# Performance work log

Measured on AMD Instinct MI355X. Metric: run time of the kernel, lower is better.

## Reference

```python
import jax, jax.numpy as jnp
import numpy as np
import math

B, T, IN_DIM = 2, 2048, 512
D, NH, MULT, N_LAYER = 512, 8, 4, 3
N = D * MULT // NH  # per-head latent dim = 256
OUT_DIM = 512
THETA = 2 ** 16


def get_freqs(n):
    t = jnp.arange(n, dtype=jnp.float32)
    q = jnp.floor(t / 2.0) * 2.0  # quantize(q=2)
    return 1.0 / (THETA ** (q / n)) / (2.0 * math.pi)


def ln(x, eps=1e-5):
    mu = jnp.mean(x, axis=-1, keepdims=True)
    var = jnp.var(x, axis=-1, keepdims=True)
    return (x - mu) * jax.lax.rsqrt(var + eps)


def rope(phases, v):
    # phases: [T, N] broadcastable to v [B, nh, T, N]
    p = (phases % 1.0) * (2.0 * math.pi)
    pc, ps = jnp.cos(p), jnp.sin(p)
    # interleave rotate: out[..., 2i] = -v[..., 2i+1], out[..., 2i+1] = v[..., 2i]
    v_rot = jnp.stack((-v[..., 1::2], v[..., ::2]), axis=-1).reshape(v.shape)
    return v * pc + v_rot * ps


def setup_inputs() -> dict:
    key = jax.random.key(0)
    ks = jax.random.split(key, 8)
    std = 0.02
    return {
        "x": jax.random.normal(ks[0], (B, T, IN_DIM), dtype=jnp.float32),
        "w_in": jax.random.normal(ks[1], (IN_DIM, D), dtype=jnp.float32) * std,
        "b_in": jnp.zeros((D,), dtype=jnp.float32),
        "encoder": jax.random.normal(ks[2], (NH, D, N), dtype=jnp.float32) * std,
        "encoder_v": jax.random.normal(ks[3], (NH, D, N), dtype=jnp.float32) * std,
        "decoder": jax.random.normal(ks[4], (NH * N, D), dtype=jnp.float32) * std,
        "head_w": jax.random.normal(ks[5], (D, OUT_DIM), dtype=jnp.float32) * std,
        "head_b": jnp.zeros((OUT_DIM,), dtype=jnp.float32),
    }


def reference(x, w_in, b_in, encoder, encoder_v, decoder, head_w, head_b):
    freqs = get_freqs(N)  # [N]
    t_idx = jnp.arange(T, dtype=jnp.float32)
    phases = t_idx[:, None] * freqs[None, :]  # [T, N]
    # strict lower-triangular causal mask (tril diagonal=-1)
    mask = (jnp.arange(T)[:, None] > jnp.arange(T)[None, :])  # [T, T]
    dec = decoder.reshape(NH, N, D)

    xs = ln(x @ w_in + b_in)  # [B, T, D]
    for _ in range(N_LAYER):
        x_res = xs
        x_sparse = jax.nn.relu(jnp.einsum('btd,hdn->bhtn', xs, encoder))  # [B,nh,T,N]
        QR = rope(phases, x_sparse)
        scores = jnp.einsum('bhtn,bhsn->bhts', QR, QR)
        scores = jnp.where(mask, scores, 0.0)
        yKV = jnp.einsum('bhts,bsd->bhtd', scores, xs)  # V = x (head-broadcast)
        yKV = ln(yKV)
        y_sparse = jax.nn.relu(jnp.einsum('bhtd,hdn->bhtn', yKV, encoder_v))
        xy_sparse = x_sparse * y_sparse  # dropout p=0 -> identity
        yMLP = jnp.einsum('bhtn,hnd->btd', xy_sparse, dec)
        xs = ln(x_res + ln(yMLP))
    logits = xs @ head_w + head_b
    return logits
```

## Files before the change

kernel.cpp:

```cpp
#include <hip/hip_runtime.h>
#include <math.h>

constexpr int B_  = 2;
constexpr int T_  = 2048;
constexpr int D_  = 512;
constexpr int NH_ = 8;
constexpr int NL_ = 256;
constexpr int HN_ = NH_ * NL_;
constexpr int BT_ = B_ * T_;

typedef __bf16 v8bf __attribute__((ext_vector_type(8)));
typedef float  v4f  __attribute__((ext_vector_type(4)));
typedef unsigned short us8 __attribute__((ext_vector_type(8)));
typedef unsigned short us4 __attribute__((ext_vector_type(4)));

__device__ inline unsigned short f2b(float f) {
    union { float f; unsigned u; } v{f};
    unsigned r = v.u + 0x7FFF + ((v.u >> 16) & 1);
    return (unsigned short)(r >> 16);
}
__device__ inline float b2f(unsigned short u) {
    union { unsigned u; float f; } v{(unsigned)u << 16};
    return v.f;
}

__device__ __forceinline__ void g2l16(const void* g, void* l) {
    __builtin_amdgcn_global_load_lds(
        (const __attribute__((address_space(1))) void*)g,
        (__attribute__((address_space(3))) void*)l, 16, 0, 0);
}

#define TILE_IDS                                              \
    int tid = threadIdx.x;                                    \
    int lane = tid & 63, wid = tid >> 6;                      \
    int wm = (wid & 1) * 64, wn = (wid >> 1) * 64;            \
    int ln16 = lane & 15, q = lane >> 4;                      \
    int srl = lane >> 2, scl = (lane & 3) * 8;                \
    (void)wm; (void)wn;

#define T128_STAGE(Ab, lda, Bb, ldb, k0, buf)                 \
    _Pragma("unroll")                                         \
    for (int ci = 0; ci < 4; ++ci) {                          \
        int c = wid * 4 + ci;                                 \
        if (c < 8) {                                          \
            int r = c * 16 + srl;                             \
            g2l16(Ab + (long)r * lda + (k0) + scl,            \
                  (char*)As[buf] + c * 1024);                 \
        } else {                                              \
            int r = (c - 8) * 16 + srl;                       \
            g2l16(Bb + (long)r * ldb + (k0) + scl,            \
                  (char*)Bs[buf] + (c - 8) * 1024);           \
        }                                                     \
    }

#define TILE_MFMA(Asx, Bsx)                                   \
    {                                                         \
        v8bf af[4], bfr[4];                                   \
        _Pragma("unroll")                                     \
        for (int r = 0; r < 4; ++r)                           \
            af[r] = *(const v8bf*)&Asx[wm + r * 16 + ln16][q * 8]; \
        _Pragma("unroll")                                     \
        for (int c = 0; c < 4; ++c)                           \
            bfr[c] = *(const v8bf*)&Bsx[wn + c * 16 + ln16][q * 8]; \
        _Pragma("unroll")                                     \
        for (int r = 0; r < 4; ++r)                           \
            _Pragma("unroll")                                 \
            for (int c = 0; c < 4; ++c)                       \
                acc[r][c] = __builtin_amdgcn_mfma_f32_16x16x32_bf16( \
                    af[r], bfr[c], acc[r][c], 0, 0, 0);       \
    }

template <int KS, bool RELU, bool MUL, bool BF16OUT, bool LNA>
__global__ __launch_bounds__(256) void gemm128(
    const unsigned short* __restrict__ A, int lda, long sA,
    const unsigned short* __restrict__ Bt, int ldb, long sB,
    void* __restrict__ Cv, int ldc, long sC,
    const unsigned short* __restrict__ mulp, int K,
    const float* __restrict__ muinv, const float* __restrict__ colsum) {
    constexpr int NHF = KS / 32;
    int m0 = blockIdx.y * 128, n0 = blockIdx.x * 128, z = blockIdx.z;
    __shared__ unsigned short As[2][NHF][128][32];
    __shared__ unsigned short Bs[2][NHF][128][32];
    const unsigned short* Ab = A  + (long)z * sA + (long)m0 * lda;
    const unsigned short* Bb = Bt + (long)z * sB + (long)n0 * ldb;
    TILE_IDS
    v4f acc[4][4] = {};
    auto stageK = [&](int k0, int buf) {
        #pragma unroll
        for (int h = 0; h < NHF; ++h)
            #pragma unroll
            for (int ci = 0; ci < 4; ++ci) {
                int c = wid * 4 + ci;
                if (c < 8)
                    g2l16(Ab + (long)(c * 16 + srl) * lda + k0 + h * 32 + scl,
                          (char*)As[buf][h] + c * 1024);
                else
                    g2l16(Bb + (long)((c - 8) * 16 + srl) * ldb + k0 + h * 32 +
                              scl,
                          (char*)Bs[buf][h] + (c - 8) * 1024);
            }
    };
    stageK(0, 0);
    __syncthreads();
    int cur = 0;
    for (int k0 = 0; k0 < K; k0 += KS) {
        if (k0 + KS < K) stageK(k0 + KS, cur ^ 1);
        #pragma unroll
        for (int h = 0; h < NHF; ++h)
            TILE_MFMA(As[cur][h], Bs[cur][h])
        __syncthreads();
        cur ^= 1;
    }
    float* Cf = (float*)Cv;
    unsigned short* Cb = (unsigned short*)Cv;
    long zoff = (long)z * sC;
    #pragma unroll
    for (int r = 0; r < 4; ++r)
        #pragma unroll
        for (int c = 0; c < 4; ++c)
            #pragma unroll
            for (int e = 0; e < 4; ++e) {
                int row = m0 + wm + r * 16 + q * 4 + e;
                int col = n0 + wn + c * 16 + ln16;
                float v = acc[r][c][e];
                if (LNA) {
                    float2 mi = *(const float2*)&muinv[((long)z * BT_ + row) * 2];
                    float cs = colsum[(long)z * NL_ + col];
                    v = mi.y * (v - mi.x * cs);
                }
                if (RELU) v = fmaxf(v, 0.f);
                long idx = zoff + (long)row * ldc + col;
                if (MUL) v *= b2f(mulp[idx]);
                if (BF16OUT) Cb[idx] = f2b(v);
                else         Cf[idx] = v;
            }
}

__global__ __launch_bounds__(256) void enc_rope(
    const unsigned short* __restrict__ A,
    const unsigned short* __restrict__ Bt,
    unsigned short* __restrict__ xsp,
    unsigned short* __restrict__ qrh,
    unsigned short* __restrict__ qrT) {
    int m0 = blockIdx.y * 128, n0 = blockIdx.x * 128;
    __shared__ unsigned short As[2][2][128][32];
    __shared__ unsigned short Bs[2][2][128][32];
    unsigned short (*lt)[68] = (unsigned short(*)[68])&As[0][0][0][0];
    const unsigned short* Ab = A + (long)m0 * 512;
    const unsigned short* Bb = Bt + (long)n0 * 512;
    TILE_IDS
    v4f acc[4][4] = {};
    auto stageK = [&](int k0, int buf) {
        #pragma unroll
        for (int h = 0; h < 2; ++h)
            #pragma unroll
            for (int ci = 0; ci < 4; ++ci) {
                int c = wid * 4 + ci;
                if (c < 8)
                    g2l16(Ab + (long)(c * 16 + srl) * 512 + k0 + h * 32 + scl,
                          (char*)As[buf][h] + c * 1024);
                else
                    g2l16(Bb + (long)((c - 8) * 16 + srl) * 512 + k0 + h * 32 +
                              scl,
                          (char*)Bs[buf][h] + (c - 8) * 1024);
            }
    };
    stageK(0, 0);
    __syncthreads();
    int cur = 0;
    for (int k0 = 0; k0 < 512; k0 += 64) {
        if (k0 + 64 < 512) stageK(k0 + 64, cur ^ 1);
        TILE_MFMA(As[cur][0], Bs[cur][0])
        TILE_MFMA(As[cur][1], Bs[cur][1])
        __syncthreads();
        cur ^= 1;
    }
    int bb = m0 >> 11;
    int tbase = m0 & (T_ - 1);
    #pragma unroll
    for (int half = 0; half < 2; ++half) {
        if (wm == half * 64) {
            #pragma unroll
            for (int r = 0; r < 4; ++r)
                #pragma unroll
                for (int c = 0; c < 4; ++c)
                    #pragma unroll
                    for (int e = 0; e < 4; ++e) {
                        int rl = wm + r * 16 + q * 4 + e;
                        int col = n0 + wn + c * 16 + ln16;
                        float v = fmaxf(acc[r][c][e], 0.f);
                        xsp[(long)(m0 + rl) * HN_ + col] = f2b(v);
                        int n = col & (NL_ - 1);
                        int n2 = n >> 1;
                        float fr = exp2f(-(float)n2 * 0.125f) *
                                   (float)(1.0 / (2.0 * M_PI));
                        float ph = (float)(tbase + rl) * fr;
                        ph = (ph - floorf(ph)) * (float)(2.0 * M_PI);
                        float s, cc;
                        __sincosf(ph, &s, &cc);
                        float vp = __shfl_xor(v, 1, 64);
                        float o = (n & 1) ? (v * cc + vp * s)
                                          : (v * cc - vp * s);
                        int hh = col >> 8;
                        qrh[((long)(bb * 8 + hh) * T_ + tbase + rl) * NL_ + n] =
                            f2b(o);
                        lt[wn + c * 16 + ln16][rl & 63] = f2b(o);
                    }
        }
        __syncthreads();
        {
            int nrow = tid >> 1, tseg = (tid & 1) * 32;
            int colg = n0 + nrow;
            int hh = colg >> 8, nn = colg & (NL_ - 1);
            long ob = ((long)(bb * 8 + hh) * NL_ + nn) * T_ + tbase +
                      half * 64 + tseg;
            #pragma unroll
            for (int u = 0; u < 8; ++u)
                *(us4*)&qrT[ob + u * 4] = *(const us4*)&lt[nrow][tseg + u * 4];
        }
        __syncthreads();
    }
}

__global__ __launch_bounds__(256) void ct_gemm(
    const unsigned short* __restrict__ xsT,
    const unsigned short* __restrict__ qrT,
    unsigned short* __restrict__ Ct) {
    int z = blockIdx.x, nt = blockIdx.y;
    int j = blockIdx.z >> 2, mt = blockIdx.z & 3;
    int b = z >> 3;
    const unsigned short* Ab =
        xsT + (long)b * D_ * T_ + (long)(mt * 128) * T_ + j * 256;
    const unsigned short* Bb =
        qrT + (long)z * NL_ * T_ + (long)(nt * 128) * T_ + j * 256;
    __shared__ unsigned short As[2][128][32];
    __shared__ unsigned short Bs[2][128][32];
    TILE_IDS
    v4f acc[4][4] = {};
    T128_STAGE(Ab, T_, Bb, T_, 0, 0)
    __syncthreads();
    int cur = 0;
    for (int k0 = 0; k0 < 256; k0 += 32) {
        if (k0 + 32 < 256) { T128_STAGE(Ab, T_, Bb, T_, k0 + 32, cur ^ 1) }
        TILE_MFMA(As[cur], Bs[cur])
        __syncthreads();
        cur ^= 1;
    }
    unsigned short* ob = Ct + ((long)z * 8 + j) * 512 * 256;
    #pragma unroll
    for (int r = 0; r < 4; ++r)
        #pragma unroll
        for (int c = 0; c < 4; ++c)
            #pragma unroll
            for (int e = 0; e < 4; ++e) {
                int row = mt * 128 + wm + r * 16 + q * 4 + e;
                int col = nt * 128 + wn + c * 16 + ln16;
                ob[(long)row * 256 + col] = f2b(acc[r][c][e]);
            }
}

__global__ __launch_bounds__(256) void prefix_k(unsigned short* __restrict__ Ct) {
    int z = blockIdx.x, dg = blockIdx.y;
    int d = dg * 8 + (threadIdx.x >> 5);
    int n0 = (threadIdx.x & 31) * 8;
    long base = ((long)z * 8) * 512 * 256 + (long)d * 256 + n0;
    constexpr long S = 512 * 256;
    us8 vals[8];
    #pragma unroll
    for (int i = 0; i < 8; ++i)
        vals[i] = *(const us8*)&Ct[base + (long)i * S];
    float acc[8] = {};
    #pragma unroll
    for (int i = 0; i < 8; ++i) {
        us8 o;
        #pragma unroll
        for (int e = 0; e < 8; ++e) o[e] = f2b(acc[e]);
        *(us8*)&Ct[base + (long)i * S] = o;
        #pragma unroll
        for (int e = 0; e < 8; ++e) acc[e] += b2f(vals[i][e]);
    }
}

__global__ __launch_bounds__(256) void sdiag(const unsigned short* __restrict__ qr,
                                             unsigned short* __restrict__ Sd) {
    int z = blockIdx.x, i = blockIdx.y, qq = blockIdx.z;
    int qm = (qq + 1) >> 1, qn = qq >> 1;
    const unsigned short* Ab =
        qr + ((long)z * T_ + i * 256 + qm * 128) * NL_;
    const unsigned short* Bb =
        qr + ((long)z * T_ + i * 256 + qn * 128) * NL_;
    bool dual = (qm != qn);
    __shared__ unsigned short As[2][128][32];
    __shared__ unsigned short Bs[2][128][32];
    TILE_IDS
    v4f acc[4][4] = {};
    auto stg = [&](int k0, int buf) {
        #pragma unroll
        for (int ci = 0; ci < 2; ++ci) {
            int c = wid * 2 + ci;
            g2l16(Ab + (long)(c * 16 + srl) * NL_ + k0 + scl,
                  (char*)As[buf] + c * 1024);
            if (dual)
                g2l16(Bb + (long)(c * 16 + srl) * NL_ + k0 + scl,
                      (char*)Bs[buf] + c * 1024);
        }
    };
    stg(0, 0);
    __syncthreads();
    int cur = 0;
    for (int k0 = 0; k0 < NL_; k0 += 32) {
        if (k0 + 32 < NL_) stg(k0 + 32, cur ^ 1);
        if (dual) { TILE_MFMA(As[cur], Bs[cur]) }
        else      { TILE_MFMA(As[cur], As[cur]) }
        __syncthreads();
        cur ^= 1;
    }
    unsigned short* ob = Sd + ((long)z * 8 + i) * 65536;
    #pragma unroll
    for (int r = 0; r < 4; ++r)
        #pragma unroll
        for (int c = 0; c < 4; ++c)
            #pragma unroll
            for (int e = 0; e < 4; ++e) {
                int row = wm + r * 16 + q * 4 + e;
                int col = wn + c * 16 + ln16;
                float v = acc[r][c][e];
                if (!dual && row <= col) v = 0.f;
                ob[(qm * 128 + row) * 256 + qn * 128 + col] = f2b(v);
            }
}

__global__ __launch_bounds__(256) void pxg(
    const unsigned short* __restrict__ qr,
    const unsigned short* __restrict__ Pt,
    const unsigned short* __restrict__ Sd,
    const unsigned short* __restrict__ xsT,
    unsigned short* __restrict__ ykvu,
    float* __restrict__ part) {
    int z = blockIdx.x, i = blockIdx.y, nt = blockIdx.z;
    int b = z >> 3, h = z & 7;
    int n0 = nt * 128;
    int i256 = i >> 1, hf2 = i & 1;
    const unsigned short* A1 = qr + ((long)z * T_ + i * 128) * NL_;
    const unsigned short* B1 =
        Pt + ((long)z * 8 + i256) * 512 * 256 + (long)n0 * 256;
    const unsigned short* A2 = Sd + ((long)z * 8 + i256) * 65536 +
                               (long)hf2 * 128 * 256;
    const unsigned short* B2 =
        xsT + (long)b * D_ * T_ + (long)n0 * T_ + i256 * 256;
    __shared__ unsigned short As[2][128][32];
    __shared__ unsigned short Bs[2][128][32];
    __shared__ float sred[128][2][2];
    TILE_IDS
    v4f acc[4][4] = {};
    int NS = 12 + hf2 * 4;
    auto stage = [&](int s) {
        const unsigned short* Ap;
        const unsigned short* Bp;
        long lda, ldb;
        int k0;
        if (s < 8) { Ap = A1; lda = NL_; Bp = B1; ldb = 256; k0 = s * 32; }
        else       { Ap = A2; lda = 256; Bp = B2; ldb = T_;  k0 = (s - 8) * 32; }
        int bi = s & 1;
        #pragma unroll
        for (int ci = 0; ci < 4; ++ci) {
            int c = wid * 4 + ci;
            if (c < 8)
                g2l16(Ap + (long)(c * 16 + srl) * lda + k0 + scl,
                      (char*)As[bi] + c * 1024);
            else
                g2l16(Bp + (long)((c - 8) * 16 + srl) * ldb + k0 + scl,
                      (char*)Bs[bi] + (c - 8) * 1024);
        }
    };
    stage(0);
    __syncthreads();
    for (int s = 0; s < NS; ++s) {
        if (s + 1 < NS) stage(s + 1);
        int bi = s & 1;
        TILE_MFMA(As[bi], Bs[bi])
        __syncthreads();
    }
    long obase = ((long)h * BT_ + (long)b * T_ + i * 128) * D_ + n0;
    #pragma unroll
    for (int r = 0; r < 4; ++r) {
        float s1[4] = {}, s2[4] = {};
        #pragma unroll
        for (int c = 0; c < 4; ++c)
            #pragma unroll
            for (int e = 0; e < 4; ++e) {
                float v = acc[r][c][e];
                s1[e] += v;
                s2[e] += v * v;
                int rl = wm + r * 16 + q * 4 + e;
                int col = wn + c * 16 + ln16;
                ykvu[obase + (long)rl * D_ + col] = f2b(v);
            }
        #pragma unroll
        for (int e = 0; e < 4; ++e) {
            #pragma unroll
            for (int off = 1; off < 16; off <<= 1) {
                s1[e] += __shfl_xor(s1[e], off, 64);
                s2[e] += __shfl_xor(s2[e], off, 64);
            }
            if (ln16 == 0) {
                int rl = wm + r * 16 + q * 4 + e;
                sred[rl][wid >> 1][0] = s1[e];
                sred[rl][wid >> 1][1] = s2[e];
            }
        }
    }
    __syncthreads();
    if (tid < 128) {
        float a = sred[tid][0][0] + sred[tid][1][0];
        float sq = sred[tid][0][1] + sred[tid][1][1];
        long pb = ((((long)z * 16 + i) * 4 + nt) * 128 + tid) * 2;
        part[pb] = a;
        part[pb + 1] = sq;
    }
}

__global__ __launch_bounds__(128) void lnstats(const float* __restrict__ part,
                                               float* __restrict__ muinv) {
    int z = blockIdx.x, i = blockIdx.y, t = threadIdx.x;
    long pb = ((((long)z * 16 + i) * 4) * 128 + t) * 2;
    float s1 = part[pb] + part[pb + 256] + part[pb + 512] + part[pb + 768];
    float s2 = part[pb + 1] + part[pb + 257] + part[pb + 513] + part[pb + 769];
    float mu = s1 * (1.0f / 512.0f);
    float var = s2 * (1.0f / 512.0f) - mu * mu;
    float inv = rsqrtf(var + 1e-5f);
    int b = z >> 3, h = z & 7;
    long row = (long)h * BT_ + (long)b * T_ + i * 128 + t;
    muinv[row * 2]     = mu;
    muinv[row * 2 + 1] = inv;
}

__global__ __launch_bounds__(256) void colsum_k(
    const unsigned short* __restrict__ encvT, float* __restrict__ cs) {
    int lane = threadIdx.x & 63, wv = threadIdx.x >> 6;
    int g = blockIdx.x * 4 + wv;
    us8 v = *(const us8*)&encvT[(long)g * 512 + lane * 8];
    float s = 0.f;
    #pragma unroll
    for (int e = 0; e < 8; ++e) s += b2f(v[e]);
    #pragma unroll
    for (int off = 1; off < 64; off <<= 1) s += __shfl_xor(s, off, 64);
    if (lane == 0) cs[g] = s;
}

__global__ __launch_bounds__(256) void trans_cast(
    const float* __restrict__ in, long sIn, unsigned short* __restrict__ out,
    long sOut, int R, int Cc) {
    __shared__ float tl[32][33];
    int z = blockIdx.z;
    int r0 = blockIdx.y * 32, c0 = blockIdx.x * 32;
    int tx = threadIdx.x & 31, ty = threadIdx.x >> 5;
    const float* ip = in + (long)z * sIn;
    unsigned short* op = out + (long)z * sOut;
    #pragma unroll
    for (int j = 0; j < 4; ++j)
        tl[ty + j * 8][tx] = ip[(long)(r0 + ty + j * 8) * Cc + c0 + tx];
    __syncthreads();
    #pragma unroll
    for (int j = 0; j < 4; ++j)
        op[(long)(c0 + ty + j * 8) * R + r0 + tx] = f2b(tl[tx][ty + j * 8]);
}

__global__ __launch_bounds__(256) void trans16(
    const unsigned short* __restrict__ in, long sIn,
    unsigned short* __restrict__ out, long sOut, int R, int Cc) {
    __shared__ unsigned short tl[32][34];
    int z = blockIdx.z;
    int r0 = blockIdx.y * 32, c0 = blockIdx.x * 32;
    int tx = threadIdx.x & 31, ty = threadIdx.x >> 5;
    const unsigned short* ip = in + (long)z * sIn;
    unsigned short* op = out + (long)z * sOut;
    #pragma unroll
    for (int j = 0; j < 4; ++j)
        tl[ty + j * 8][tx] = ip[(long)(r0 + ty + j * 8) * Cc + c0 + tx];
    __syncthreads();
    #pragma unroll
    for (int j = 0; j < 4; ++j)
        op[(long)(c0 + ty + j * 8) * R + r0 + tx] = tl[tx][ty + j * 8];
}

__global__ __launch_bounds__(256) void cast_b(const float* __restrict__ in,
                                              unsigned short* __restrict__ out) {
    long i = ((long)blockIdx.x * 256 + threadIdx.x) * 4;
    float4 v = *(const float4*)&in[i];
    ushort4 o;
    o.x = f2b(v.x); o.y = f2b(v.y); o.z = f2b(v.z); o.w = f2b(v.w);
    *(ushort4*)&out[i] = o;
}

__global__ __launch_bounds__(256) void add_out4(const float* __restrict__ t,
                                                long slice,
                                                const float* __restrict__ bias,
                                                float* __restrict__ o) {
    long i = ((long)blockIdx.x * 256 + threadIdx.x) * 4;
    float4 v0 = *(const float4*)&t[i];
    float4 v1 = *(const float4*)&t[i + slice];
    float4 v2 = *(const float4*)&t[i + 2 * slice];
    float4 v3 = *(const float4*)&t[i + 3 * slice];
    float4 bv = *(const float4*)&bias[i & 511];
    float4 r;
    r.x = v0.x + v1.x + v2.x + v3.x + bv.x;
    r.y = v0.y + v1.y + v2.y + v3.y + bv.y;
    r.z = v0.z + v1.z + v2.z + v3.z + bv.z;
    r.w = v0.w + v1.w + v2.w + v3.w + bv.w;
    *(float4*)&o[i] = r;
}

__device__ inline float2 block_reduce2(float a, float b) {
    __shared__ float sa[4], sb[4];
    #pragma unroll
    for (int off = 32; off; off >>= 1) {
        a += __shfl_down(a, off, 64);
        b += __shfl_down(b, off, 64);
    }
    __syncthreads();
    int w = threadIdx.x >> 6;
    if ((threadIdx.x & 63) == 0) { sa[w] = a; sb[w] = b; }
    __syncthreads();
    return make_float2(sa[0] + sa[1] + sa[2] + sa[3],
                       sb[0] + sb[1] + sb[2] + sb[3]);
}
__device__ inline float2 ln_pair(float2 v) {
    float2 s = block_reduce2(v.x + v.y, 0.f);
    float mu = s.x * (1.0f / 512.0f);
    float dx = v.x - mu, dy = v.y - mu;
    float2 q = block_reduce2(dx * dx + dy * dy, 0.f);
    float inv = rsqrtf(q.x * (1.0f / 512.0f) + 1e-5f);
    return make_float2(dx * inv, dy * inv);
}

__global__ __launch_bounds__(256) void ln_dual4(const float* __restrict__ t,
                                                long slice,
                                                const float* __restrict__ bias,
                                                float* __restrict__ outf,
                                                unsigned short* __restrict__ outb) {
    long row = blockIdx.x;
    int c = threadIdx.x * 2;
    long i = row * 512 + c;
    float2 v0 = *(const float2*)&t[i];
    float2 v1 = *(const float2*)&t[i + slice];
    float2 v2 = *(const float2*)&t[i + 2 * slice];
    float2 v3 = *(const float2*)&t[i + 3 * slice];
    float2 bv = *(const float2*)&bias[c];
    float2 v = make_float2(v0.x + v1.x + v2.x + v3.x + bv.x,
                           v0.y + v1.y + v2.y + v3.y + bv.y);
    float2 o = ln_pair(v);
    *(float2*)&outf[i] = o;
    ushort2 ob; ob.x = f2b(o.x); ob.y = f2b(o.y);
    *(ushort2*)&outb[i] = ob;
}

__global__ __launch_bounds__(256) void combine_dual4(
    const float* __restrict__ t, long slice, const float* __restrict__ xres,
    float* __restrict__ outf, unsigned short* __restrict__ outb) {
    long row = blockIdx.x;
    int c = threadIdx.x * 2;
    long i = row * 512 + c;
    float2 v0 = *(const float2*)&t[i];
    float2 v1 = *(const float2*)&t[i + slice];
    float2 v2 = *(const float2*)&t[i + 2 * slice];
    float2 v3 = *(const float2*)&t[i + 3 * slice];
    float2 y = make_float2(v0.x + v1.x + v2.x + v3.x,
                           v0.y + v1.y + v2.y + v3.y);
    float2 l = ln_pair(y);
    float2 r = *(const float2*)&xres[i];
    float2 z = make_float2(r.x + l.x, r.y + l.y);
    float2 o = ln_pair(z);
    *(float2*)&outf[i] = o;
    ushort2 ob; ob.x = f2b(o.x); ob.y = f2b(o.y);
    *(ushort2*)&outb[i] = ob;
}

extern "C" void kernel_launch(void* const* d_in, const int* in_sizes, int n_in,
                              void* d_out, int out_size, void* d_ws,
                              size_t ws_size, hipStream_t stream) {
    const float* x      = (const float*)d_in[0];
    const float* w_in   = (const float*)d_in[1];
    const float* b_in   = (const float*)d_in[2];
    const float* enc    = (const float*)d_in[3];
    const float* enc_v  = (const float*)d_in[4];
    const float* dec    = (const float*)d_in[5];
    const float* head_w = (const float*)d_in[6];
    const float* head_b = (const float*)d_in[7];
    float* out = (float*)d_out;

    char* w = (char*)d_ws;
    auto alloc = [&](size_t bytes) { void* p = (void*)w; w += bytes; return p; };
    unsigned short* w_inT = (unsigned short*)alloc((size_t)512 * 512 * 2);
    unsigned short* headT = (unsigned short*)alloc((size_t)512 * 512 * 2);
    unsigned short* encT  = (unsigned short*)alloc((size_t)NH_ * NL_ * D_ * 2);
    unsigned short* encvT = (unsigned short*)alloc((size_t)NH_ * NL_ * D_ * 2);
    unsigned short* decT  = (unsigned short*)alloc((size_t)D_ * HN_ * 2);
    unsigned short* xb    = (unsigned short*)alloc((size_t)BT_ * D_ * 2);
    float*          tmp   = (float*)alloc((size_t)4 * BT_ * D_ * 4);
    float*          xsf0  = (float*)alloc((size_t)BT_ * D_ * 4);
    float*          xsf1  = (float*)alloc((size_t)BT_ * D_ * 4);
    unsigned short* xs_b  = (unsigned short*)alloc((size_t)BT_ * D_ * 2);
    unsigned short* xsT   = (unsigned short*)alloc((size_t)B_ * D_ * T_ * 2);
    unsigned short* xsp   = (unsigned short*)alloc((size_t)BT_ * HN_ * 2);
    unsigned short* qrh   = (unsigned short*)alloc((size_t)BT_ * HN_ * 2);
    unsigned short* qrT   = (unsigned short*)alloc((size_t)BT_ * HN_ * 2);
    unsigned short* Ct    = (unsigned short*)alloc((size_t)128 * 512 * 256 * 2);
    unsigned short* Sd    = (unsigned short*)alloc((size_t)128 * 256 * 256 * 2);
    unsigned short* ykv   = (unsigned short*)alloc((size_t)NH_ * BT_ * D_ * 2);
    float*          part  = (float*)alloc((size_t)256 * 4 * 128 * 2 * 4);
    float*          muinv = (float*)alloc((size_t)NH_ * BT_ * 2 * 4);
    float*          csum  = (float*)alloc((size_t)HN_ * 4);
    const long SL = (long)BT_ * D_;

    cast_b<<<BT_ * D_ / 1024, 256, 0, stream>>>(x, xb);
    trans_cast<<<dim3(16, 16, 1), 256, 0, stream>>>(w_in, 0, w_inT, 0, 512, 512);
    trans_cast<<<dim3(16, 16, 1), 256, 0, stream>>>(head_w, 0, headT, 0, 512, 512);
    trans_cast<<<dim3(8, 16, 8), 256, 0, stream>>>(enc, (long)D_ * NL_, encT,
                                                   (long)NL_ * D_, D_, NL_);
    trans_cast<<<dim3(8, 16, 8), 256, 0, stream>>>(enc_v, (long)D_ * NL_, encvT,
                                                   (long)NL_ * D_, D_, NL_);
    trans_cast<<<dim3(16, 64, 1), 256, 0, stream>>>(dec, 0, decT, 0, HN_, D_);
    colsum_k<<<HN_ / 4, 256, 0, stream>>>(encvT, csum);

    gemm128<64, false, false, false, false>
        <<<dim3(4, 32, 4), 256, 0, stream>>>(xb, D_, 128, w_inT, D_, 128, tmp,
                                             D_, SL, nullptr, 128, nullptr,
                                             nullptr);
    ln_dual4<<<BT_, 256, 0, stream>>>(tmp, SL, b_in, xsf0, xs_b);
    trans16<<<dim3(16, 64, 2), 256, 0, stream>>>(xs_b, (long)T_ * D_, xsT,
                                                 (long)D_ * T_, T_, D_);

    float* xin = xsf0;
    float* xout = xsf1;
    for (int l = 0; l < 3; ++l) {
        enc_rope<<<dim3(16, 32), 256, 0, stream>>>(xs_b, encT, xsp, qrh, qrT);
        ct_gemm<<<dim3(16, 2, 32), 256, 0, stream>>>(xsT, qrT, Ct);
        prefix_k<<<dim3(16, 64), 256, 0, stream>>>(Ct);
        sdiag<<<dim3(16, 8, 3), 256, 0, stream>>>(qrh, Sd);
        pxg<<<dim3(16, 16, 4), 256, 0, stream>>>(qrh, Ct, Sd, xsT, ykv, part);
        lnstats<<<dim3(16, 16), 128, 0, stream>>>(part, muinv);
        gemm128<64, true, true, true, true>
            <<<dim3(2, 32, 8), 256, 0, stream>>>(
                ykv, D_, (long)BT_ * D_, encvT, D_, (long)NL_ * D_, xsp, HN_,
                NL_, xsp, 512, muinv, csum);
        gemm128<64, false, false, false, false>
            <<<dim3(4, 32, 4), 256, 0, stream>>>(
                xsp, HN_, 512, decT, HN_, 512, tmp, D_, SL, nullptr, 512,
                nullptr, nullptr);
        combine_dual4<<<BT_, 256, 0, stream>>>(tmp, SL, xin, xout, xs_b);
        trans16<<<dim3(16, 64, 2), 256, 0, stream>>>(xs_b, (long)T_ * D_, xsT,
                                                     (long)D_ * T_, T_, D_);
        float* t = xin; xin = xout; xout = t;
    }

    gemm128<64, false, false, false, false>
        <<<dim3(4, 32, 4), 256, 0, stream>>>(xs_b, D_, 128, headT, D_, 128, tmp,
                                             D_, SL, nullptr, 128, nullptr,
                                             nullptr);
    add_out4<<<BT_ * 512 / 1024, 256, 0, stream>>>(tmp, SL, head_b, out);
}
```

Baseline: 591.9 us.

## Pipeline enc_rope K-loop with 4-stage async buffers and single-pass transpose epilogue

```diff
diff --git a/kernel.cpp b/kernel.cpp
--- a/kernel.cpp
+++ b/kernel.cpp
@@ -143,82 +143,75 @@
     unsigned short* __restrict__ qrh,
     unsigned short* __restrict__ qrT) {
     int m0 = blockIdx.y * 128, n0 = blockIdx.x * 128;
-    __shared__ unsigned short As[2][2][128][32];
-    __shared__ unsigned short Bs[2][2][128][32];
-    unsigned short (*lt)[68] = (unsigned short(*)[68])&As[0][0][0][0];
+    __shared__ unsigned short As[4][128][32];
+    __shared__ unsigned short Bs[4][128][32];
+    unsigned short (*lt)[136] = (unsigned short(*)[136])&As[0][0][0];
     const unsigned short* Ab = A + (long)m0 * 512;
     const unsigned short* Bb = Bt + (long)n0 * 512;
     TILE_IDS
     v4f acc[4][4] = {};
-    auto stageK = [&](int k0, int buf) {
-        #pragma unroll
-        for (int h = 0; h < 2; ++h)
-            #pragma unroll
-            for (int ci = 0; ci < 4; ++ci) {
-                int c = wid * 4 + ci;
-                if (c < 8)
-                    g2l16(Ab + (long)(c * 16 + srl) * 512 + k0 + h * 32 + scl,
-                          (char*)As[buf][h] + c * 1024);
-                else
-                    g2l16(Bb + (long)((c - 8) * 16 + srl) * 512 + k0 + h * 32 +
-                              scl,
-                          (char*)Bs[buf][h] + (c - 8) * 1024);
-            }
+    auto stage = [&](int t) {
+        int k0 = t * 32, buf = t & 3;
+        #pragma unroll
+        for (int ci = 0; ci < 4; ++ci) {
+            int c = wid * 4 + ci;
+            if (c < 8)
+                g2l16(Ab + (long)(c * 16 + srl) * 512 + k0 + scl,
+                      (char*)As[buf] + c * 1024);
+            else
+                g2l16(Bb + (long)((c - 8) * 16 + srl) * 512 + k0 + scl,
+                      (char*)Bs[buf] + (c - 8) * 1024);
+        }
     };
-    stageK(0, 0);
-    __syncthreads();
-    int cur = 0;
-    for (int k0 = 0; k0 < 512; k0 += 64) {
-        if (k0 + 64 < 512) stageK(k0 + 64, cur ^ 1);
-        TILE_MFMA(As[cur][0], Bs[cur][0])
-        TILE_MFMA(As[cur][1], Bs[cur][1])
-        __syncthreads();
-        cur ^= 1;
-    }
+    stage(0);
+    stage(1);
+#define ER_STEP(T, VM)                                          \
+    asm volatile("s_waitcnt vmcnt(" VM ")" ::: "memory");       \
+    __builtin_amdgcn_s_barrier();                               \
+    asm volatile("" ::: "memory");                              \
+    if ((T) + 2 < 16) stage((T) + 2);                           \
+    TILE_MFMA(As[(T) & 3], Bs[(T) & 3])
+    ER_STEP(0, "4")  ER_STEP(1, "4")  ER_STEP(2, "4")  ER_STEP(3, "4")
+    ER_STEP(4, "4")  ER_STEP(5, "4")  ER_STEP(6, "4")  ER_STEP(7, "4")
+    ER_STEP(8, "4")  ER_STEP(9, "4")  ER_STEP(10, "4") ER_STEP(11, "4")
+    ER_STEP(12, "4") ER_STEP(13, "4") ER_STEP(14, "4") ER_STEP(15, "0")
+#undef ER_STEP
+    __syncthreads();
     int bb = m0 >> 11;
     int tbase = m0 & (T_ - 1);
     #pragma unroll
-    for (int half = 0; half < 2; ++half) {
-        if (wm == half * 64) {
+    for (int r = 0; r < 4; ++r)
+        #pragma unroll
+        for (int c = 0; c < 4; ++c)
             #pragma unroll
-            for (int r = 0; r < 4; ++r)
-                #pragma unroll
-                for (int c = 0; c < 4; ++c)
-                    #pragma unroll
-                    for (int e = 0; e < 4; ++e) {
-                        int rl = wm + r * 16 + q * 4 + e;
-                        int col = n0 + wn + c * 16 + ln16;
-                        float v = fmaxf(acc[r][c][e], 0.f);
-                        xsp[(long)(m0 + rl) * HN_ + col] = f2b(v);
-                        int n = col & (NL_ - 1);
-                        int n2 = n >> 1;
-                        float fr = exp2f(-(float)n2 * 0.125f) *
-                                   (float)(1.0 / (2.0 * M_PI));
-                        float ph = (float)(tbase + rl) * fr;
-                        ph = (ph - floorf(ph)) * (float)(2.0 * M_PI);
-                        float s, cc;
-                        __sincosf(ph, &s, &cc);
-                        float vp = __shfl_xor(v, 1, 64);
-                        float o = (n & 1) ? (v * cc + vp * s)
-                                          : (v * cc - vp * s);
-                        int hh = col >> 8;
-                        qrh[((long)(bb * 8 + hh) * T_ + tbase + rl) * NL_ + n] =
-                            f2b(o);
-                        lt[wn + c * 16 + ln16][rl & 63] = f2b(o);
-                    }
-        }
-        __syncthreads();
-        {
-            int nrow = tid >> 1, tseg = (tid & 1) * 32;
-            int colg = n0 + nrow;
-            int hh = colg >> 8, nn = colg & (NL_ - 1);
-            long ob = ((long)(bb * 8 + hh) * NL_ + nn) * T_ + tbase +
-                      half * 64 + tseg;
-            #pragma unroll
-            for (int u = 0; u < 8; ++u)
-                *(us4*)&qrT[ob + u * 4] = *(const us4*)&lt[nrow][tseg + u * 4];
-        }
-        __syncthreads();
+            for (int e = 0; e < 4; ++e) {
+                int rl = wm + r * 16 + q * 4 + e;
+                int col = n0 + wn + c * 16 + ln16;
+                float v = fmaxf(acc[r][c][e], 0.f);
+                xsp[(long)(m0 + rl) * HN_ + col] = f2b(v);
+                int n = col & (NL_ - 1);
+                int n2 = n >> 1;
+                float fr = exp2f(-(float)n2 * 0.125f) *
+                           (float)(1.0 / (2.0 * M_PI));
+                float ph = (float)(tbase + rl) * fr;
+                ph = (ph - floorf(ph)) * (float)(2.0 * M_PI);
+                float s, cc;
+                __sincosf(ph, &s, &cc);
+                float vp = __shfl_xor(v, 1, 64);
+                float o = (n & 1) ? (v * cc + vp * s) : (v * cc - vp * s);
+                int hh = col >> 8;
+                qrh[((long)(bb * 8 + hh) * T_ + tbase + rl) * NL_ + n] = f2b(o);
+                lt[wn + c * 16 + ln16][rl] = f2b(o);
+            }
+    __syncthreads();
+    {
+        int nrow = tid >> 1, tseg = (tid & 1) * 64;
+        int colg = n0 + nrow;
+        int hh = colg >> 8, nn = colg & (NL_ - 1);
+        long ob = ((long)(bb * 8 + hh) * NL_ + nn) * T_ + tbase + tseg;
+        #pragma unroll
+        for (int u = 0; u < 16; ++u)
+            *(us4*)&qrT[ob + u * 4] = *(const us4*)&lt[nrow][tseg + u * 4];
     }
 }
 
```

Result: no change. 581.8 us (-1.7%).
